# Kernel optimization log

Measured on AMD Instinct MI355X. Metric: run time of the kernel, lower is better.

The kernel has to match this reference:

```python
import jax, jax.numpy as jnp
import numpy as np

# --- config mirroring Prediction(__init__) ---
NUM_CLS = 3        # heatmap channels; total C = NUM_CLS + 2 (offset) + 2 (wh)
TOPK = 100         # peaks kept per stack output
SCALE = 4.0        # scale_factor: feature-map stride
CONF_TH = 0.1      # conf_th (also soft-NMS keep thresh, as in forward())
SIGMA = 0.5        # soft-NMS gaussian sigma (default in soft_nms_pytorch)


def setup_inputs() -> dict:
    key = jax.random.key(0)
    # network is identity => x is the raw head output (B, S, C, H, W)
    x = jax.random.normal(key, (32, 2, NUM_CLS + 4, 256, 256), dtype=jnp.float32)
    return {"x": x}


def _decode(hm, off, wh):
    """CenterNet-style hm2box: hm (C,H,W) post-sigmoid, off/wh (2,H,W)."""
    C, H, W = hm.shape
    scores, idx = jax.lax.top_k(hm.reshape(-1), TOPK)      # over C*H*W
    cls = idx // (H * W)
    rem = idx % (H * W)                                    # spatial flat index
    ys = (rem // W).astype(jnp.float32)
    xs = (rem % W).astype(jnp.float32)
    offx = off[0].reshape(-1)[rem]
    offy = off[1].reshape(-1)[rem]
    bw = wh[0].reshape(-1)[rem] * SCALE
    bh = wh[1].reshape(-1)[rem] * SCALE
    cx = (xs + offx) * SCALE
    cy = (ys + offy) * SCALE
    boxes = jnp.stack([cx - bw / 2, cy - bh / 2, cx + bw / 2, cy + bh / 2], axis=-1)
    # conf_th filter: zero-out low scores (fixed shape stand-in for boolean select)
    scores = jnp.where(scores > CONF_TH, scores, 0.0)
    return boxes, cls, scores


def _soft_nms(boxes, scores):
    """Faithful port of soft_nms_pytorch: sequential max-swap + gaussian decay."""
    N = boxes.shape[0]
    pos = jnp.arange(N)

    def step(carry, i):
        bxs, scs, idxs = carry
        # argmax over scores[i:] (includes i; strict '<' in original == first-max here)
        m = jnp.argmax(jnp.where(pos >= i, scs, -jnp.inf))

        def swap(a):
            ai, am = a[i], a[m]
            return a.at[i].set(am).at[m].set(ai)

        bxs, scs, idxs = swap(bxs), swap(scs), swap(idxs)
        bi = bxs[i]
        x1, y1, x2, y2 = bxs[:, 0], bxs[:, 1], bxs[:, 2], bxs[:, 3]
        areas = (x2 - x1 + 1.0) * (y2 - y1 + 1.0)
        area_i = (bi[2] - bi[0] + 1.0) * (bi[3] - bi[1] + 1.0)
        xx1 = jnp.maximum(bi[0], x1)
        yy1 = jnp.maximum(bi[1], y1)
        xx2 = jnp.minimum(bi[2], x2)
        yy2 = jnp.minimum(bi[3], y2)
        inter = jnp.maximum(0.0, xx2 - xx1 + 1.0) * jnp.maximum(0.0, yy2 - yy1 + 1.0)
        iou = inter / (area_i + areas - inter)
        w = jnp.exp(-(iou * iou) / SIGMA)
        scs = jnp.where(pos > i, w * scs, scs)   # decay only positions after i
        return (bxs, scs, idxs), None

    (bxs, scs, idxs), _ = jax.lax.scan(step, (boxes, scores, jnp.arange(N)), jnp.arange(N))
    keep = scs > CONF_TH
    return bxs, scs, idxs, keep


def reference(x):
    b, s, c, H, W = x.shape
    hm = jax.nn.sigmoid(x[:, :, :NUM_CLS])
    off = x[:, :, NUM_CLS:NUM_CLS + 2]
    wh = x[:, :, NUM_CLS + 2:]
    boxes, clss, scores = jax.vmap(jax.vmap(_decode))(hm, off, wh)
    boxes = boxes.reshape(b, s * TOPK, 4)
    clss = clss.reshape(b, s * TOPK)
    scores = scores.reshape(b, s * TOPK)
    nboxes, nscores, idxs, keep = jax.vmap(_soft_nms)(boxes, scores)
    nclss = jnp.take_along_axis(clss, idxs, axis=1)
    # fixed-shape outputs; `keep` marks the boxes the original would return
    return nboxes, nclss, nscores, keep
```

## Files before the change

kernel.cpp:

```cpp
#include <hip/hip_runtime.h>
#include <math.h>

#define TOPK 100
#define HW 65536
#define SLICE_STRIDE (7*HW)
#define NBATCH 32
#define NBOX 200
#define HM (3*HW)
#define CAP 4096
#define CCAP 2048
#define WS_NEED ((size_t)(192 * TOPK * 8))
#define TKEY 0xC0200000u

__device__ __forceinline__ unsigned fkey(float f) {
    unsigned u = __float_as_uint(f);
    return (u & 0x80000000u) ? ~u : (u | 0x80000000u);
}

#if defined(__has_builtin) && __has_builtin(__builtin_amdgcn_update_dpp)
#define DPP64_STEP(ctrl)                                                        \
    {                                                                           \
        unsigned lo = (unsigned)x, hi = (unsigned)(x >> 32);                    \
        unsigned olo = (unsigned)__builtin_amdgcn_update_dpp((int)lo, (int)lo,  \
                                                             (ctrl), 0xF, 0xF, false); \
        unsigned ohi = (unsigned)__builtin_amdgcn_update_dpp((int)hi, (int)hi,  \
                                                             (ctrl), 0xF, 0xF, false); \
        unsigned long long o = ((unsigned long long)ohi << 32) | olo;           \
        x = (o > x) ? o : x;                                                    \
    }
__device__ __forceinline__ unsigned long long wave_umax64(unsigned long long x) {
    DPP64_STEP(0x111)
    DPP64_STEP(0x112)
    DPP64_STEP(0x114)
    DPP64_STEP(0x118)
    DPP64_STEP(0x142)
    DPP64_STEP(0x143)
    unsigned rlo = (unsigned)__builtin_amdgcn_readlane((int)(unsigned)x, 63);
    unsigned rhi = (unsigned)__builtin_amdgcn_readlane((int)(unsigned)(x >> 32), 63);
    return ((unsigned long long)rhi << 32) | rlo;
}
#else
__device__ __forceinline__ unsigned long long wave_umax64(unsigned long long x) {
    #pragma unroll
    for (int off = 32; off > 0; off >>= 1) {
        unsigned long long o = __shfl_xor(x, off);
        if (o > x) x = o;
    }
    return x;
}
#endif

__global__ __launch_bounds__(1024) void kcol(const float* __restrict__ x,
                                             unsigned long long* __restrict__ ws) {
    __shared__ unsigned long long cand[CCAP];
    __shared__ unsigned hist[4096];
    __shared__ int shB, shB2;
    __shared__ unsigned shAbove, shNcand, shNc;

    const int bid = blockIdx.x;
    const int slice = bid / 3, c = bid % 3;
    const int t = threadIdx.x;
    const float* xc = x + (size_t)slice * SLICE_STRIDE + (size_t)c * HW;
    const float4* xc4 = (const float4*)xc;
    const int N4 = HW / 4;
    const unsigned cbase = (unsigned)c << 16;

    if (t == 0) shNc = 0u;
    __syncthreads();

    #pragma unroll 4
    for (int i = t; i < N4; i += 1024) {
        float4 v = xc4[i];
        float a[4] = {v.x, v.y, v.z, v.w};
        #pragma unroll
        for (int q = 0; q < 4; ++q) {
            unsigned vk = fkey(a[q]);
            if (vk >= TKEY) {
                unsigned pos = atomicAdd(&shNc, 1u);
                if (pos < CCAP)
                    cand[pos] = ((unsigned long long)vk << 32) |
                                (unsigned)~(cbase | (unsigned)(i * 4 + q));
            }
        }
    }
    __syncthreads();
    unsigned nc = shNc;

    if (nc < TOPK || nc > CCAP) {
        if (t == 0) { shB = 0; shB2 = 0; shAbove = 0u; shNcand = 0u; shNc = 0u; }
        for (int i = t; i < 4096; i += 1024) hist[i] = 0u;
        __syncthreads();
        for (int i = t; i < N4; i += 1024) {
            float4 v = xc4[i];
            float a[4] = {v.x, v.y, v.z, v.w};
            #pragma unroll
            for (int q = 0; q < 4; ++q) atomicAdd(&hist[fkey(a[q]) >> 20], 1u);
        }
        __syncthreads();
        {
            unsigned* tmp = (unsigned*)cand;
            unsigned* src = hist;
            unsigned* dst = tmp;
            for (int d = 1; d < 4096; d <<= 1) {
                for (int i = t; i < 4096; i += 1024) {
                    unsigned v2 = src[i];
                    if (i + d < 4096) v2 += src[i + d];
                    dst[i] = v2;
                }
                __syncthreads();
                unsigned* sw = src; src = dst; dst = sw;
            }
            for (int i = t; i < 4096; i += 1024) {
                unsigned sb = src[i];
                unsigned sn = (i < 4095) ? src[i + 1] : 0u;
                if (sb >= TOPK && sn < TOPK) { shB = i; shAbove = sn; shNcand = sb; }
            }
            __syncthreads();
        }
        const bool refine = (shNcand > CCAP);
        if (refine) {
            for (int i = t; i < 4096; i += 1024) hist[i] = 0u;
            __syncthreads();
            const unsigned Bv = (unsigned)shB;
            for (int i = t; i < N4; i += 1024) {
                float4 v = xc4[i];
                float a[4] = {v.x, v.y, v.z, v.w};
                #pragma unroll
                for (int q = 0; q < 4; ++q) {
                    unsigned vk = fkey(a[q]);
                    if ((vk >> 20) == Bv) atomicAdd(&hist[(vk >> 8) & 0xFFFu], 1u);
                }
            }
            __syncthreads();
            if (t == 0) {
                unsigned need = TOPK - shAbove, cum = 0u;
                int b2 = 4095;
                for (; b2 >= 0; --b2) { cum += hist[b2]; if (cum >= need) break; }
                shB2 = (b2 < 0) ? 0 : b2;
            }
            __syncthreads();
        }
        {
            const unsigned Bv = (unsigned)shB;
            const unsigned B2v = refine ? (unsigned)shB2 : 0u;
            for (int i = t; i < N4; i += 1024) {
                float4 v = xc4[i];
                float a[4] = {v.x, v.y, v.z, v.w};
                #pragma unroll
                for (int q = 0; q < 4; ++q) {
                    unsigned vk = fkey(a[q]);
                    unsigned bin = vk >> 20;
                    bool ok = refine ? (bin > Bv || (bin == Bv && ((vk >> 8) & 0xFFFu) >= B2v))
                                     : (bin >= Bv);
                    if (ok) {
                        unsigned pos = atomicAdd(&shNc, 1u);
                        if (pos < CCAP)
                            cand[pos] = ((unsigned long long)vk << 32) |
                                        (unsigned)~(cbase | (unsigned)(i * 4 + q));
                    }
                }
            }
            __syncthreads();
        }
        nc = shNc; if (nc > CCAP) nc = CCAP;
    }

    int P = 128; while (P < (int)nc) P <<= 1;
    for (int i = (int)nc + t; i < P; i += 1024) cand[i] = 0ull;
    __syncthreads();
    for (int k = 2; k <= P; k <<= 1) {
        for (int j = k >> 1; j > 0; j >>= 1) {
            for (int i = t; i < P; i += 1024) {
                int ixj = i ^ j;
                if (ixj > i) {
                    unsigned long long a = cand[i], c2 = cand[ixj];
                    bool sw = ((i & k) == 0) ? (a < c2) : (a > c2);
                    if (sw) { cand[i] = c2; cand[ixj] = a; }
                }
            }
            __syncthreads();
        }
    }

    if (t < TOPK) ws[(size_t)bid * TOPK + t] = cand[t];
}

__global__ __launch_bounds__(512) void knms4(const float* __restrict__ x,
                                             const unsigned long long* __restrict__ ws,
                                             float* __restrict__ out) {
    __shared__ unsigned long long skey[2][512];
    __shared__ float4 bxs4[NBOX];
    __shared__ float scs[NBOX];
    __shared__ float cl[NBOX];

    const int b = blockIdx.x, t = threadIdx.x;
    const int half = t >> 8, tt = t & 255;
    const int slice = 2 * b + half;

    for (int i = tt; i < 512; i += 256)
        skey[half][i] = (i < 3 * TOPK) ? ws[(size_t)slice * 3 * TOPK + i] : 0ull;
    __syncthreads();
    for (int k = 2; k <= 512; k <<= 1) {
        for (int j = k >> 1; j > 0; j >>= 1) {
            for (int i = tt; i < 512; i += 256) {
                int ixj = i ^ j;
                if (ixj > i) {
                    unsigned long long a = skey[half][i], c2 = skey[half][ixj];
                    bool sw = ((i & k) == 0) ? (a < c2) : (a > c2);
                    if (sw) { skey[half][i] = c2; skey[half][ixj] = a; }
                }
            }
            __syncthreads();
        }
    }
    if (tt < TOPK) {
        unsigned long long K = skey[half][tt];
        unsigned vk = (unsigned)(K >> 32);
        unsigned idx = ~((unsigned)K);
        unsigned u = (vk & 0x80000000u) ? (vk & 0x7FFFFFFFu) : ~vk;
        float z = __uint_as_float(u);
        int c = (int)(idx >> 16);
        int rem = (int)(idx & 0xFFFFu);
        const float* xb = x + (size_t)slice * SLICE_STRIDE;
        float ysf = (float)(rem >> 8);
        float xsf = (float)(rem & 255);
        float offx = xb[3 * HW + rem];
        float offy = xb[4 * HW + rem];
        float bw = xb[5 * HW + rem] * 4.0f;
        float bh = xb[6 * HW + rem] * 4.0f;
        float cx = (xsf + offx) * 4.0f;
        float cy = (ysf + offy) * 4.0f;
        int slot = half * TOPK + tt;
        bxs4[slot] = make_float4(cx - bw * 0.5f, cy - bh * 0.5f,
                                 cx + bw * 0.5f, cy + bh * 0.5f);
        float sg = 1.0f / (1.0f + expf(-z));
        scs[slot] = (sg > 0.1f) ? sg : 0.0f;
        cl[slot] = (float)c;
    }
    __syncthreads();

    if (t < 64) {
        float X1[4], Y1[4], X2[4], Y2[4], SC[4], CL4[4], AR[4];
        unsigned CP[4];
        #pragma unroll
        for (int sl = 0; sl < 4; ++sl) {
            int p = sl * 64 + t;
            int q = (p < NBOX) ? p : 0;
            float4 bb = bxs4[q];
            X1[sl] = bb.x; Y1[sl] = bb.y; X2[sl] = bb.z; Y2[sl] = bb.w;
            SC[sl] = (p < NBOX) ? scs[q] : 0.0f;
            CL4[sl] = cl[q];
            CP[sl] = (unsigned)p;
            AR[sl] = (X2[sl] - X1[sl] + 1.0f) * (Y2[sl] - Y1[sl] + 1.0f);
        }

        for (int i = 0; i < NBOX; ++i) {
            const unsigned ui = (unsigned)i;
            unsigned long long loc = 0ull;
            #pragma unroll
            for (int sl = 0; sl < 4; ++sl) {
                int p = sl * 64 + t;
                unsigned cd = ~((CP[sl] << 8) | (unsigned)p);
                unsigned long long k =
                    ((unsigned long long)__float_as_uint(SC[sl]) << 32) | cd;
                if (CP[sl] >= ui && k > loc) loc = k;
            }
            unsigned long long kmax = wave_umax64(loc);
            unsigned w32 = ~((unsigned)kmax);
            unsigned m = w32 >> 8;
            unsigned worig = w32 & 0xFFu;

            float4 pv = bxs4[worig];
            float area_i = (pv.z - pv.x + 1.0f) * (pv.w - pv.y + 1.0f);

            #pragma unroll
            for (int sl = 0; sl < 4; ++sl) {
                unsigned cp = CP[sl];
                unsigned ncp = (cp == ui) ? m : cp;
                ncp = (cp == m) ? ui : ncp;
                CP[sl] = ncp;
            }

            #pragma unroll
            for (int sl = 0; sl < 4; ++sl) {
                int p = sl * 64 + t;
                if ((p < NBOX) && (CP[sl] > ui)) {
                    float x1 = X1[sl], y1 = Y1[sl], x2 = X2[sl], y2 = Y2[sl];
                    float xx1 = fmaxf(pv.x, x1);
                    float yy1 = fmaxf(pv.y, y1);
                    float xx2 = fminf(pv.z, x2);
                    float yy2 = fminf(pv.w, y2);
                    float inter = fmaxf(0.0f, xx2 - xx1 + 1.0f) *
                                  fmaxf(0.0f, yy2 - yy1 + 1.0f);
                    float iou = inter / (area_i + AR[sl] - inter);
                    float w = expf(-(iou * iou) / 0.5f);
                    SC[sl] = w * SC[sl];
                }
            }
        }

        float* ob  = out + (size_t)b * NBOX * 4;
        float* oc  = out + (size_t)NBATCH * NBOX * 4 + b * NBOX;
        float* os  = out + (size_t)NBATCH * NBOX * 5 + b * NBOX;
        float* okp = out + (size_t)NBATCH * NBOX * 6 + b * NBOX;
        #pragma unroll
        for (int sl = 0; sl < 4; ++sl) {
            int p = sl * 64 + t;
            if (p < NBOX) {
                unsigned q = CP[sl];
                ob[q * 4 + 0] = X1[sl];
                ob[q * 4 + 1] = Y1[sl];
                ob[q * 4 + 2] = X2[sl];
                ob[q * 4 + 3] = Y2[sl];
                oc[q]  = CL4[sl];
                os[q]  = SC[sl];
                okp[q] = (SC[sl] > 0.1f) ? 1.0f : 0.0f;
            }
        }
    }
}

__global__ __launch_bounds__(1024) void ktopk(const float* __restrict__ x,
                                              float* __restrict__ out) {
    __shared__ unsigned hist[4096];
    __shared__ unsigned long long cand[CAP];
    __shared__ int shB, shB2;
    __shared__ unsigned shAbove, shNcand, shNc;

    const int slice = blockIdx.x;
    const int b = slice >> 1, s = slice & 1;
    const int t = threadIdx.x;
    const float* xb = x + (size_t)slice * SLICE_STRIDE;
    const float4* xb4 = (const float4*)xb;
    const int N4 = HM / 4;

    if (t == 0) { shB = 0; shB2 = 0; shAbove = 0u; shNcand = 0u; shNc = 0u; }
    for (int i = t; i < 4096; i += 1024) hist[i] = 0u;
    __syncthreads();

    for (int i = t; i < N4; i += 1024) {
        float4 v = xb4[i];
        float a[4] = {v.x, v.y, v.z, v.w};
        #pragma unroll
        for (int c_ = 0; c_ < 4; ++c_) {
            unsigned vk = fkey(a[c_]);
            atomicAdd(&hist[vk >> 20], 1u);
        }
    }
    __syncthreads();

    {
        unsigned* tmp = (unsigned*)cand;
        unsigned* src = hist;
        unsigned* dst = tmp;
        for (int d = 1; d < 4096; d <<= 1) {
            for (int i = t; i < 4096; i += 1024) {
                unsigned v = src[i];
                if (i + d < 4096) v += src[i + d];
                dst[i] = v;
            }
            __syncthreads();
            unsigned* sw = src; src = dst; dst = sw;
        }
        for (int i = t; i < 4096; i += 1024) {
            unsigned sb = src[i];
            unsigned sn = (i < 4095) ? src[i + 1] : 0u;
            if (sb >= TOPK && sn < TOPK) { shB = i; shAbove = sn; shNcand = sb; }
        }
        __syncthreads();
    }

    const bool refine = (shNcand > CAP);
    if (refine) {
        for (int i = t; i < 4096; i += 1024) hist[i] = 0u;
        __syncthreads();
        const unsigned Bv = (unsigned)shB;
        for (int i = t; i < N4; i += 1024) {
            float4 v = xb4[i];
            float a[4] = {v.x, v.y, v.z, v.w};
            #pragma unroll
            for (int c_ = 0; c_ < 4; ++c_) {
                unsigned vk = fkey(a[c_]);
                if ((vk >> 20) == Bv) atomicAdd(&hist[(vk >> 8) & 0xFFFu], 1u);
            }
        }
        __syncthreads();
        if (t == 0) {
            unsigned need = TOPK - shAbove, cum = 0u;
            int b2 = 4095;
            for (; b2 >= 0; --b2) { cum += hist[b2]; if (cum >= need) break; }
            shB2 = (b2 < 0) ? 0 : b2;
            shNcand = shAbove + cum;
        }
        __syncthreads();
    }

    {
        const unsigned Bv = (unsigned)shB;
        const unsigned B2v = refine ? (unsigned)shB2 : 0u;
        for (int i = t; i < N4; i += 1024) {
            float4 v = xb4[i];
            float a[4] = {v.x, v.y, v.z, v.w};
            #pragma unroll
            for (int c_ = 0; c_ < 4; ++c_) {
                unsigned vk = fkey(a[c_]);
                unsigned bin = vk >> 20;
                bool q = refine ? (bin > Bv || (bin == Bv && ((vk >> 8) & 0xFFFu) >= B2v))
                                : (bin >= Bv);
                if (q) {
                    unsigned pos = atomicAdd(&shNc, 1u);
                    if (pos < CAP)
                        cand[pos] = ((unsigned long long)vk << 32) |
                                    (unsigned)~(unsigned)(i * 4 + c_);
                }
            }
        }
        __syncthreads();
    }

    unsigned nc = shNc; if (nc > CAP) nc = CAP;
    int P = 128; while (P < (int)nc) P <<= 1;
    for (int i = (int)nc + t; i < P; i += 1024) cand[i] = 0ull;
    __syncthreads();
    for (int k = 2; k <= P; k <<= 1) {
        for (int j = k >> 1; j > 0; j >>= 1) {
            for (int i = t; i < P; i += 1024) {
                int ixj = i ^ j;
                if (ixj > i) {
                    unsigned long long a = cand[i], c2 = cand[ixj];
                    bool sw = ((i & k) == 0) ? (a < c2) : (a > c2);
                    if (sw) { cand[i] = c2; cand[ixj] = a; }
                }
            }
            __syncthreads();
        }
    }

    if (t < TOPK) {
        unsigned long long K = cand[t];
        unsigned vk = (unsigned)(K >> 32);
        unsigned idx = ~((unsigned)K);
        unsigned u = (vk & 0x80000000u) ? (vk & 0x7FFFFFFFu) : ~vk;
        float z = __uint_as_float(u);
        int c = (int)(idx >> 16);
        int rem = (int)(idx & 0xFFFFu);
        float ysf = (float)(rem >> 8);
        float xsf = (float)(rem & 255);
        float offx = xb[3 * HW + rem];
        float offy = xb[4 * HW + rem];
        float bw = xb[5 * HW + rem] * 4.0f;
        float bh = xb[6 * HW + rem] * 4.0f;
        float cx = (xsf + offx) * 4.0f;
        float cy = (ysf + offy) * 4.0f;
        int slot = s * TOPK + t;
        float* ob = out + (size_t)b * NBOX * 4;
        float* oc = out + (size_t)NBATCH * NBOX * 4 + b * NBOX;
        float* os = out + (size_t)NBATCH * NBOX * 5 + b * NBOX;
        ob[slot * 4 + 0] = cx - bw * 0.5f;
        ob[slot * 4 + 1] = cy - bh * 0.5f;
        ob[slot * 4 + 2] = cx + bw * 0.5f;
        ob[slot * 4 + 3] = cy + bh * 0.5f;
        float sg = 1.0f / (1.0f + expf(-z));
        os[slot] = (sg > 0.1f) ? sg : 0.0f;
        oc[slot] = (float)c;
    }
}

__global__ __launch_bounds__(64) void knms(float* __restrict__ out) {
    __shared__ float bxs[NBOX][4];
    __shared__ float scs[NBOX];
    __shared__ float cl[NBOX];

    const int b = blockIdx.x, t = threadIdx.x;
    float* ob  = out + (size_t)b * NBOX * 4;
    float* oc  = out + (size_t)NBATCH * NBOX * 4 + b * NBOX;
    float* os  = out + (size_t)NBATCH * NBOX * 5 + b * NBOX;
    float* okp = out + (size_t)NBATCH * NBOX * 6 + b * NBOX;

    for (int p = t; p < NBOX; p += 64) {
        bxs[p][0] = ob[p * 4 + 0];
        bxs[p][1] = ob[p * 4 + 1];
        bxs[p][2] = ob[p * 4 + 2];
        bxs[p][3] = ob[p * 4 + 3];
        scs[p] = os[p];
        cl[p]  = oc[p];
    }
    __syncthreads();

    unsigned long long local = 0ull;
    for (int p = t; p < NBOX; p += 64) {
        unsigned long long k =
            ((unsigned long long)__float_as_uint(scs[p]) << 32) | (unsigned)~(unsigned)p;
        if (k > local) local = k;
    }
    #pragma unroll
    for (int off = 32; off > 0; off >>= 1) {
        unsigned long long o = __shfl_xor(local, off);
        if (o > local) local = o;
    }
    unsigned long long kmax = local;

    for (int i = 0; i < NBOX; ++i) {
        int m = (int)(~((unsigned)kmax));
        if (t == 0 && m != i) {
            #pragma unroll
            for (int k = 0; k < 4; ++k) {
                float tmp = bxs[i][k]; bxs[i][k] = bxs[m][k]; bxs[m][k] = tmp;
            }
            float ts = scs[i]; scs[i] = scs[m]; scs[m] = ts;
            float tc = cl[i];  cl[i]  = cl[m];  cl[m]  = tc;
        }
        __syncthreads();

        float b0 = bxs[i][0], b1 = bxs[i][1], b2 = bxs[i][2], b3 = bxs[i][3];
        float area_i = (b2 - b0 + 1.0f) * (b3 - b1 + 1.0f);

        local = 0ull;
        for (int p = i + 1 + t; p < NBOX; p += 64) {
            float x1 = bxs[p][0], y1 = bxs[p][1], x2 = bxs[p][2], y2 = bxs[p][3];
            float areas = (x2 - x1 + 1.0f) * (y2 - y1 + 1.0f);
            float xx1 = fmaxf(b0, x1);
            float yy1 = fmaxf(b1, y1);
            float xx2 = fminf(b2, x2);
            float yy2 = fminf(b3, y2);
            float inter = fmaxf(0.0f, xx2 - xx1 + 1.0f) * fmaxf(0.0f, yy2 - yy1 + 1.0f);
            float iou = inter / (area_i + areas - inter);
            float w = expf(-(iou * iou) / 0.5f);
            float ns = w * scs[p];
            scs[p] = ns;
            unsigned long long k =
                ((unsigned long long)__float_as_uint(ns) << 32) | (unsigned)~(unsigned)p;
            if (k > local) local = k;
        }
        __syncthreads();
        #pragma unroll
        for (int off = 32; off > 0; off >>= 1) {
            unsigned long long o = __shfl_xor(local, off);
            if (o > local) local = o;
        }
        kmax = local;
    }
    __syncthreads();

    for (int p = t; p < NBOX; p += 64) {
        ob[p * 4 + 0] = bxs[p][0];
        ob[p * 4 + 1] = bxs[p][1];
        ob[p * 4 + 2] = bxs[p][2];
        ob[p * 4 + 3] = bxs[p][3];
        oc[p]  = cl[p];
        os[p]  = scs[p];
        okp[p] = (scs[p] > 0.1f) ? 1.0f : 0.0f;
    }
}

extern "C" void kernel_launch(void* const* d_in, const int* in_sizes, int n_in,
                              void* d_out, int out_size, void* d_ws, size_t ws_size,
                              hipStream_t stream) {
    const float* x = (const float*)d_in[0];
    float* out = (float*)d_out;
    if (d_ws != nullptr && ws_size >= WS_NEED) {
        kcol<<<192, 1024, 0, stream>>>(x, (unsigned long long*)d_ws);
        knms4<<<NBATCH, 512, 0, stream>>>(x, (const unsigned long long*)d_ws, out);
    } else {
        ktopk<<<2 * NBATCH, 1024, 0, stream>>>(x, out);
        knms<<<NBATCH, 64, 0, stream>>>(out);
    }
}
```

Measured before the change: 312.5 us.

## Select top-k per slice in one block and simplify soft-NMS broadcast

Top-k selection now runs in one block per (batch, stack) slice over all three heatmap channels, instead of one block per channel followed by a merge sort in the NMS kernel. The NMS kernel drops the 512-key bitonic merge, shrinks to 256 threads, and reads the selected box from registers via readlane instead of shared memory. It also exits the soft-NMS loop early once the remaining maximum score is zero. The cost is that only 64 blocks each scan three times as much data, which lowers parallelism in the memory-bound scan stage. A higher threshold (TKEYS) keeps the candidate count bounded.

```diff
diff --git a/kernel.cpp b/kernel.cpp
--- a/kernel.cpp
+++ b/kernel.cpp
@@ -8,13 +8,21 @@
 #define NBOX 200
 #define HM (3*HW)
 #define CAP 4096
-#define CCAP 2048
-#define WS_NEED ((size_t)(192 * TOPK * 8))
-#define TKEY 0xC0200000u
+#define SCAP 2048
+#define WS_NEED ((size_t)(64 * TOPK * 8))
+#define TKEYS 0xC0400000u
 
 __device__ __forceinline__ unsigned fkey(float f) {
     unsigned u = __float_as_uint(f);
     return (u & 0x80000000u) ? ~u : (u | 0x80000000u);
+}
+
+__device__ __forceinline__ float sel4(const float a[4], int s) {
+    float r = a[0];
+    r = (s == 1) ? a[1] : r;
+    r = (s == 2) ? a[2] : r;
+    r = (s == 3) ? a[3] : r;
+    return r;
 }
 
 #if defined(__has_builtin) && __has_builtin(__builtin_amdgcn_update_dpp)
@@ -39,6 +47,10 @@
     unsigned rhi = (unsigned)__builtin_amdgcn_readlane((int)(unsigned)(x >> 32), 63);
     return ((unsigned long long)rhi << 32) | rlo;
 }
+__device__ __forceinline__ float lane_getf(const float a[4], int slot, int lane) {
+    return __uint_as_float((unsigned)__builtin_amdgcn_readlane(
+        (int)__float_as_uint(sel4(a, slot)), lane));
+}
 #else
 __device__ __forceinline__ unsigned long long wave_umax64(unsigned long long x) {
     #pragma unroll
@@ -48,50 +60,51 @@
     }
     return x;
 }
+__device__ __forceinline__ float lane_getf(const float a[4], int slot, int lane) {
+    return __shfl(sel4(a, slot), lane);
+}
 #endif
 
-__global__ __launch_bounds__(1024) void kcol(const float* __restrict__ x,
-                                             unsigned long long* __restrict__ ws) {
-    __shared__ unsigned long long cand[CCAP];
+__global__ __launch_bounds__(1024) void kslice(const float* __restrict__ x,
+                                               unsigned long long* __restrict__ ws) {
+    __shared__ unsigned long long cand[SCAP];
     __shared__ unsigned hist[4096];
     __shared__ int shB, shB2;
     __shared__ unsigned shAbove, shNcand, shNc;
 
-    const int bid = blockIdx.x;
-    const int slice = bid / 3, c = bid % 3;
+    const int slice = blockIdx.x;
     const int t = threadIdx.x;
-    const float* xc = x + (size_t)slice * SLICE_STRIDE + (size_t)c * HW;
-    const float4* xc4 = (const float4*)xc;
-    const int N4 = HW / 4;
-    const unsigned cbase = (unsigned)c << 16;
+    const float* xb = x + (size_t)slice * SLICE_STRIDE;
+    const float4* xb4 = (const float4*)xb;
+    const int N4 = HM / 4;
 
     if (t == 0) shNc = 0u;
     __syncthreads();
 
     #pragma unroll 4
     for (int i = t; i < N4; i += 1024) {
-        float4 v = xc4[i];
+        float4 v = xb4[i];
         float a[4] = {v.x, v.y, v.z, v.w};
         #pragma unroll
         for (int q = 0; q < 4; ++q) {
             unsigned vk = fkey(a[q]);
-            if (vk >= TKEY) {
+            if (vk >= TKEYS) {
                 unsigned pos = atomicAdd(&shNc, 1u);
-                if (pos < CCAP)
+                if (pos < SCAP)
                     cand[pos] = ((unsigned long long)vk << 32) |
-                                (unsigned)~(cbase | (unsigned)(i * 4 + q));
+                                (unsigned)~(unsigned)(i * 4 + q);
             }
         }
     }
     __syncthreads();
     unsigned nc = shNc;
 
-    if (nc < TOPK || nc > CCAP) {
+    if (nc < TOPK || nc > SCAP) {
         if (t == 0) { shB = 0; shB2 = 0; shAbove = 0u; shNcand = 0u; shNc = 0u; }
         for (int i = t; i < 4096; i += 1024) hist[i] = 0u;
         __syncthreads();
         for (int i = t; i < N4; i += 1024) {
-            float4 v = xc4[i];
+            float4 v = xb4[i];
             float a[4] = {v.x, v.y, v.z, v.w};
             #pragma unroll
             for (int q = 0; q < 4; ++q) atomicAdd(&hist[fkey(a[q]) >> 20], 1u);
@@ -117,13 +130,13 @@
             }
             __syncthreads();
         }
-        const bool refine = (shNcand > CCAP);
+        const bool refine = (shNcand > SCAP);
         if (refine) {
             for (int i = t; i < 4096; i += 1024) hist[i] = 0u;
             __syncthreads();
             const unsigned Bv = (unsigned)shB;
             for (int i = t; i < N4; i += 1024) {
-                float4 v = xc4[i];
+                float4 v = xb4[i];
                 float a[4] = {v.x, v.y, v.z, v.w};
                 #pragma unroll
                 for (int q = 0; q < 4; ++q) {
@@ -144,7 +157,7 @@
             const unsigned Bv = (unsigned)shB;
             const unsigned B2v = refine ? (unsigned)shB2 : 0u;
             for (int i = t; i < N4; i += 1024) {
-                float4 v = xc4[i];
+                float4 v = xb4[i];
                 float a[4] = {v.x, v.y, v.z, v.w};
                 #pragma unroll
                 for (int q = 0; q < 4; ++q) {
@@ -154,15 +167,15 @@
                                      : (bin >= Bv);
                     if (ok) {
                         unsigned pos = atomicAdd(&shNc, 1u);
-                        if (pos < CCAP)
+                        if (pos < SCAP)
                             cand[pos] = ((unsigned long long)vk << 32) |
-                                        (unsigned)~(cbase | (unsigned)(i * 4 + q));
+                                        (unsigned)~(unsigned)(i * 4 + q);
                     }
                 }
             }
             __syncthreads();
         }
-        nc = shNc; if (nc > CCAP) nc = CCAP;
+        nc = shNc; if (nc > SCAP) nc = SCAP;
     }
 
     int P = 128; while (P < (int)nc) P <<= 1;
@@ -182,39 +195,22 @@
         }
     }
 
-    if (t < TOPK) ws[(size_t)bid * TOPK + t] = cand[t];
-}
-
-__global__ __launch_bounds__(512) void knms4(const float* __restrict__ x,
+    if (t < TOPK) ws[(size_t)slice * TOPK + t] = cand[t];
+}
+
+__global__ __launch_bounds__(256) void knms5(const float* __restrict__ x,
                                              const unsigned long long* __restrict__ ws,
                                              float* __restrict__ out) {
-    __shared__ unsigned long long skey[2][512];
     __shared__ float4 bxs4[NBOX];
     __shared__ float scs[NBOX];
     __shared__ float cl[NBOX];
 
     const int b = blockIdx.x, t = threadIdx.x;
-    const int half = t >> 8, tt = t & 255;
-    const int slice = 2 * b + half;
-
-    for (int i = tt; i < 512; i += 256)
-        skey[half][i] = (i < 3 * TOPK) ? ws[(size_t)slice * 3 * TOPK + i] : 0ull;
-    __syncthreads();
-    for (int k = 2; k <= 512; k <<= 1) {
-        for (int j = k >> 1; j > 0; j >>= 1) {
-            for (int i = tt; i < 512; i += 256) {
-                int ixj = i ^ j;
-                if (ixj > i) {
-                    unsigned long long a = skey[half][i], c2 = skey[half][ixj];
-                    bool sw = ((i & k) == 0) ? (a < c2) : (a > c2);
-                    if (sw) { skey[half][i] = c2; skey[half][ixj] = a; }
-                }
-            }
-            __syncthreads();
-        }
-    }
-    if (tt < TOPK) {
-        unsigned long long K = skey[half][tt];
+
+    if (t < NBOX) {
+        const int s = t / TOPK, rank = t - s * TOPK;
+        const int slice = 2 * b + s;
+        unsigned long long K = ws[(size_t)slice * TOPK + rank];
         unsigned vk = (unsigned)(K >> 32);
         unsigned idx = ~((unsigned)K);
         unsigned u = (vk & 0x80000000u) ? (vk & 0x7FFFFFFFu) : ~vk;
@@ -230,12 +226,11 @@
         float bh = xb[6 * HW + rem] * 4.0f;
         float cx = (xsf + offx) * 4.0f;
         float cy = (ysf + offy) * 4.0f;
-        int slot = half * TOPK + tt;
-        bxs4[slot] = make_float4(cx - bw * 0.5f, cy - bh * 0.5f,
-                                 cx + bw * 0.5f, cy + bh * 0.5f);
+        bxs4[t] = make_float4(cx - bw * 0.5f, cy - bh * 0.5f,
+                              cx + bw * 0.5f, cy + bh * 0.5f);
         float sg = 1.0f / (1.0f + expf(-z));
-        scs[slot] = (sg > 0.1f) ? sg : 0.0f;
-        cl[slot] = (float)c;
+        scs[t] = (sg > 0.1f) ? sg : 0.0f;
+        cl[t] = (float)c;
     }
     __syncthreads();
 
@@ -259,19 +254,25 @@
             unsigned long long loc = 0ull;
             #pragma unroll
             for (int sl = 0; sl < 4; ++sl) {
-                int p = sl * 64 + t;
-                unsigned cd = ~((CP[sl] << 8) | (unsigned)p);
+                unsigned cd = ~((CP[sl] << 8) | (unsigned)(sl * 64 + t));
                 unsigned long long k =
                     ((unsigned long long)__float_as_uint(SC[sl]) << 32) | cd;
                 if (CP[sl] >= ui && k > loc) loc = k;
             }
             unsigned long long kmax = wave_umax64(loc);
+
+            if ((unsigned)(kmax >> 32) == 0u) break;
+
             unsigned w32 = ~((unsigned)kmax);
             unsigned m = w32 >> 8;
-            unsigned worig = w32 & 0xFFu;
-
-            float4 pv = bxs4[worig];
-            float area_i = (pv.z - pv.x + 1.0f) * (pv.w - pv.y + 1.0f);
+            int worig = (int)(w32 & 0xFFu);
+            int lane_m = worig & 63, slot_m = worig >> 6;
+
+            float pvx1 = lane_getf(X1, slot_m, lane_m);
+            float pvy1 = lane_getf(Y1, slot_m, lane_m);
+            float pvx2 = lane_getf(X2, slot_m, lane_m);
+            float pvy2 = lane_getf(Y2, slot_m, lane_m);
+            float area_i = lane_getf(AR, slot_m, lane_m);
 
             #pragma unroll
             for (int sl = 0; sl < 4; ++sl) {
@@ -286,10 +287,10 @@
                 int p = sl * 64 + t;
                 if ((p < NBOX) && (CP[sl] > ui)) {
                     float x1 = X1[sl], y1 = Y1[sl], x2 = X2[sl], y2 = Y2[sl];
-                    float xx1 = fmaxf(pv.x, x1);
-                    float yy1 = fmaxf(pv.y, y1);
-                    float xx2 = fminf(pv.z, x2);
-                    float yy2 = fminf(pv.w, y2);
+                    float xx1 = fmaxf(pvx1, x1);
+                    float yy1 = fmaxf(pvy1, y1);
+                    float xx2 = fminf(pvx2, x2);
+                    float yy2 = fminf(pvy2, y2);
                     float inter = fmaxf(0.0f, xx2 - xx1 + 1.0f) *
                                   fmaxf(0.0f, yy2 - yy1 + 1.0f);
                     float iou = inter / (area_i + AR[sl] - inter);
@@ -559,8 +560,8 @@
     const float* x = (const float*)d_in[0];
     float* out = (float*)d_out;
     if (d_ws != nullptr && ws_size >= WS_NEED) {
-        kcol<<<192, 1024, 0, stream>>>(x, (unsigned long long*)d_ws);
-        knms4<<<NBATCH, 512, 0, stream>>>(x, (const unsigned long long*)d_ws, out);
+        kslice<<<2 * NBATCH, 1024, 0, stream>>>(x, (unsigned long long*)d_ws);
+        knms5<<<NBATCH, 256, 0, stream>>>(x, (const unsigned long long*)d_ws, out);
     } else {
         ktopk<<<2 * NBATCH, 1024, 0, stream>>>(x, out);
         knms<<<NBATCH, 64, 0, stream>>>(out);
```

After: 341.1 us. 9.2% more time.
